# Optimization experiments

Hardware: AMD Instinct MI355X
Metric: run time of the kernel (lower is better)

## Reference

```python
import jax, jax.numpy as jnp
import numpy as np

N_HEADS, D_MODEL, D_HEAD = 16, 1024, 64
BATCH, SEQ = 8, 1024
INIT_RANGE = 0.02
IGNORE = -100000.0


def setup_inputs() -> dict:
    key = jax.random.key(0)
    ks = jax.random.split(key, 6)
    return {
        "normalized_resid_pre": jax.random.normal(ks[0], (BATCH, SEQ, D_MODEL), jnp.float32),
        "encoder_output": jax.random.normal(ks[1], (BATCH, SEQ, D_MODEL), jnp.float32),
        "Qs": jax.random.normal(ks[2], (N_HEADS, D_MODEL, D_HEAD), jnp.float32) * INIT_RANGE,
        "Qbs": jnp.zeros((N_HEADS, D_HEAD), jnp.float32),
        "Ks": jax.random.normal(ks[3], (N_HEADS, D_MODEL, D_HEAD), jnp.float32) * INIT_RANGE,
        "Kbs": jnp.zeros((N_HEADS, D_HEAD), jnp.float32),
        "Vs": jax.random.normal(ks[4], (N_HEADS, D_MODEL, D_HEAD), jnp.float32) * INIT_RANGE,
        "Vbs": jnp.zeros((N_HEADS, D_HEAD), jnp.float32),
        "O": jax.random.normal(ks[5], (N_HEADS, D_HEAD, D_MODEL), jnp.float32) * INIT_RANGE,
        "Ob": jnp.zeros((D_MODEL,), jnp.float32),
    }


def reference(normalized_resid_pre, encoder_output, Qs, Qbs, Ks, Kbs, Vs, Vbs, O, Ob):
    sqrt_d_head = np.sqrt(D_HEAD).astype(np.float32)
    # per-head projections: q,k from encoder_output, v from normalized_resid_pre
    q = jnp.einsum('bpd,hdk->bphk', encoder_output, Qs) + Qbs
    k = jnp.einsum('bpd,hdk->bphk', encoder_output, Ks) + Kbs
    v = jnp.einsum('bpd,hdk->bphk', normalized_resid_pre, Vs) + Vbs
    # [B,H,Q,K] scores, scaled then causally masked with -1e5 (not -inf)
    scores = jnp.einsum('bqhk,bmhk->bhqm', q, k) / sqrt_d_head
    causal = jnp.triu(jnp.ones((SEQ, SEQ), bool), k=1)
    scores = jnp.where(causal, jnp.float32(IGNORE), scores)
    attn = jax.nn.softmax(scores, axis=-1)
    z = jnp.einsum('bmhk,bhqm->bqhk', v, attn)
    return jnp.einsum('bqhk,hkd->bqd', z, O) + Ob
```

## Files before the change

### kernel.cpp

```cpp
#include <hip/hip_runtime.h>
#include <hip/hip_bf16.h>
#include <cstdint>
#include <cstddef>
#include <math.h>


typedef __attribute__((ext_vector_type(8))) short short8;
typedef __attribute__((ext_vector_type(4))) short short4v;
typedef __attribute__((ext_vector_type(4))) float f32x4;

#define MFMA16(A, B, C) __builtin_amdgcn_mfma_f32_16x16x32_bf16(A, B, C, 0, 0, 0)

__device__ inline short f2bs(float f) {
    __bf16 h = (__bf16)f;
    return __builtin_bit_cast(short, h);
}

typedef const __attribute__((address_space(1))) unsigned int* as1_u32p;
typedef __attribute__((address_space(3))) unsigned int* as3_u32p;

__device__ inline void gload_lds16(const void* g, void* lds_base) {
    __builtin_amdgcn_global_load_lds((as1_u32p)(uintptr_t)g,
                                     (as3_u32p)(uintptr_t)lds_base, 16, 0, 0);
}

__global__ __launch_bounds__(256) void cvt_k(const float* __restrict__ a,
                                             const float* __restrict__ b,
                                             short* __restrict__ oa,
                                             short* __restrict__ ob) {
    const int n = 8 * 1024 * 1024;
    const float* src = blockIdx.y ? b : a;
    short* dst = blockIdx.y ? ob : oa;
    for (int i = (blockIdx.x * 256 + threadIdx.x) * 8; i < n; i += gridDim.x * 256 * 8) {
        f32x4 v0 = *(const f32x4*)(src + i), v1 = *(const f32x4*)(src + i + 4);
        short8 o;
        o[0] = f2bs(v0[0]); o[1] = f2bs(v0[1]); o[2] = f2bs(v0[2]); o[3] = f2bs(v0[3]);
        o[4] = f2bs(v1[0]); o[5] = f2bs(v1[1]); o[6] = f2bs(v1[2]); o[7] = f2bs(v1[3]);
        *(short8*)(dst + i) = o;
    }
}

__global__ __launch_bounds__(256) void wtrans_k(
    const float* __restrict__ Wq, const float* __restrict__ Wk,
    const float* __restrict__ Wv, const float* __restrict__ Wo,
    short* __restrict__ TQ, short* __restrict__ TK,
    short* __restrict__ TV, short* __restrict__ TO) {
    __shared__ short tile[64][72];
    const int wsel = blockIdx.y;
    const float* in = wsel == 0 ? Wq : wsel == 1 ? Wk : wsel == 2 ? Wv : Wo;
    short* out = wsel == 0 ? TQ : wsel == 1 ? TK : wsel == 2 ? TV : TO;
    const int h = blockIdx.x >> 4, tk = blockIdx.x & 15;
    const int t = threadIdx.x;
    size_t ioff; int istr, orow0, ocol0;
    if (wsel < 3) { ioff = (size_t)h * 65536 + (size_t)tk * 64 * 64; istr = 64;   orow0 = h * 64;  ocol0 = tk * 64; }
    else          { ioff = (size_t)h * 65536 + (size_t)tk * 64;      istr = 1024; orow0 = tk * 64; ocol0 = h * 64; }
    {
        const int r = t >> 2, c0 = (t & 3) * 16;
        const float* src = in + ioff + (size_t)r * istr + c0;
#pragma unroll
        for (int j = 0; j < 4; j++) {
            f32x4 v = *(const f32x4*)(src + j * 4);
            tile[r][c0 + j * 4 + 0] = f2bs(v[0]);
            tile[r][c0 + j * 4 + 1] = f2bs(v[1]);
            tile[r][c0 + j * 4 + 2] = f2bs(v[2]);
            tile[r][c0 + j * 4 + 3] = f2bs(v[3]);
        }
    }
    __syncthreads();
    {
        const int cc = t >> 2, rb = (t & 3) * 16;
        short8 o0, o1;
#pragma unroll
        for (int j = 0; j < 8; j++) { o0[j] = tile[rb + j][cc]; o1[j] = tile[rb + 8 + j][cc]; }
        short* dst = out + (size_t)(orow0 + cc) * 1024 + ocol0 + rb;
        *(short8*)dst = o0;
        *(short8*)(dst + 8) = o1;
    }
}

template <int MODE>
__global__ __launch_bounds__(256) void gemm_bt(const short* __restrict__ A,
                                               const short* __restrict__ B,
                                               const float* __restrict__ bias,
                                               void* __restrict__ Cp,
                                               const float* __restrict__ bias2,
                                               void* __restrict__ Cp2) {
    constexpr int K = 1024;
    __shared__ short As[128 * 64];
    __shared__ short Bs[128 * 64];
    const int t = threadIdx.x, l = t & 63, w = t >> 6, lr = l & 15, lg = l >> 4;
    const int wm = (w >> 1) * 64, wn = (w & 1) * 64;
    const int m0 = blockIdx.x * 128, n0 = blockIdx.y * 128;
    const int sr = l >> 3, cb = l & 7;
    f32x4 acc[4][4] = {};

    for (int k0 = 0; k0 < K; k0 += 64) {
#pragma unroll
        for (int i = 0; i < 4; i++) {
            const int c = w * 4 + i, r = c * 8 + sr, cbs = cb ^ (r & 7);
            gload_lds16(A + (size_t)(m0 + r) * K + k0 + cbs * 8, &As[c * 512]);
        }
#pragma unroll
        for (int i = 0; i < 4; i++) {
            const int c = w * 4 + i, r = c * 8 + sr, cbs = cb ^ (r & 7);
            gload_lds16(B + (size_t)(n0 + r) * K + k0 + cbs * 8, &Bs[c * 512]);
        }
        __syncthreads();
#pragma unroll
        for (int kk = 0; kk < 2; kk++) {
            short8 af[4], bf[4];
#pragma unroll
            for (int mi = 0; mi < 4; mi++) {
                const int r = wm + mi * 16 + lr;
                af[mi] = *(const short8*)&As[r * 64 + ((kk * 4 + lg) ^ (r & 7)) * 8];
            }
#pragma unroll
            for (int nj = 0; nj < 4; nj++) {
                const int r = wn + nj * 16 + lr;
                bf[nj] = *(const short8*)&Bs[r * 64 + ((kk * 4 + lg) ^ (r & 7)) * 8];
            }
#pragma unroll
            for (int mi = 0; mi < 4; mi++)
#pragma unroll
                for (int nj = 0; nj < 4; nj++)
                    acc[mi][nj] = MFMA16(af[mi], bf[nj], acc[mi][nj]);
        }
        __syncthreads();
    }

#pragma unroll
    for (int mi = 0; mi < 4; mi++) {
#pragma unroll
        for (int nj = 0; nj < 4; nj++) {
            const int col = n0 + wn + nj * 16 + lr;
            if (MODE == 3) {
                const int h2 = col >> 6;
                short* dst = (short*)(h2 < 16 ? Cp : Cp2);
                const float bv = h2 < 16 ? bias[col & 1023] : bias2[col & 1023];
                const int h = h2 & 15, d = col & 63;
#pragma unroll
                for (int e = 0; e < 4; e++) {
                    const int row = m0 + wm + mi * 16 + lg * 4 + e;
                    const int bb = row >> 10, s = row & 1023;
                    dst[((size_t)(bb * 16 + h) * 1024 + s) * 64 + d] =
                        f2bs(acc[mi][nj][e] + bv);
                }
            } else if (MODE == 2) {
                const float bv = bias[col];
                const int rowb = m0 + wm + mi * 16 + lg * 4;
                const int bb = rowb >> 10, s0 = rowb & 1023;
                const int h = col >> 6, d = col & 63;
                short4v pk;
#pragma unroll
                for (int e = 0; e < 4; e++) pk[e] = f2bs(acc[mi][nj][e] + bv);
                *(short4v*)((short*)Cp + ((size_t)(bb * 16 + h) * 64 + d) * 1024 + s0) = pk;
            } else {
                const float bv = bias[col];
#pragma unroll
                for (int e = 0; e < 4; e++) {
                    const int row = m0 + wm + mi * 16 + lg * 4 + e;
                    ((float*)Cp)[(size_t)row * 1024 + col] = acc[mi][nj][e] + bv;
                }
            }
        }
    }
}

#define ATTN_THR 11.5415603f

__device__ __forceinline__ void attn_tile(
    const short* __restrict__ Ks, const short* __restrict__ Vt,
    short (*__restrict__ Psw)[76],
    const short8* __restrict__ qf, float* __restrict__ m,
    float* __restrict__ ps, f32x4* __restrict__ acc,
    bool diag, int lr, int lg, int rowloc) {
    f32x4 sf[4];
#pragma unroll
    for (int n = 0; n < 4; n++) {
        const int rk = n * 16 + lr;
        short8 kf0 = *(const short8*)&Ks[rk * 64 + ((lg) ^ (rk & 7)) * 8];
        short8 kf1 = *(const short8*)&Ks[rk * 64 + ((4 + lg) ^ (rk & 7)) * 8];
        f32x4 s = {};
        s = MFMA16(qf[0], kf0, s);
        s = MFMA16(qf[1], kf1, s);
        sf[n] = s;
    }
    const float SC = 0.18033688f;
#pragma unroll
    for (int n = 0; n < 4; n++)
#pragma unroll
        for (int e = 0; e < 4; e++) {
            float x = sf[n][e] * SC;
            if (diag && (n * 16 + lr > rowloc + e)) x = -1e30f;
            sf[n][e] = x;
        }
    float pm[4];
#pragma unroll
    for (int e = 0; e < 4; e++)
        pm[e] = fmaxf(fmaxf(sf[0][e], sf[1][e]), fmaxf(sf[2][e], sf[3][e]));
    bool ok = true;
#pragma unroll
    for (int e = 0; e < 4; e++) ok = ok && (pm[e] <= m[e] + ATTN_THR);
    if (!__all(ok)) {
#pragma unroll
        for (int e = 0; e < 4; e++) {
            float tm = pm[e];
#pragma unroll
            for (int off = 1; off < 16; off <<= 1)
                tm = fmaxf(tm, __shfl_xor(tm, off));
            float nm = fmaxf(m[e], tm);
            float al = exp2f(m[e] - nm);
            m[e] = nm;
            ps[e] *= al;
#pragma unroll
            for (int n4 = 0; n4 < 4; n4++) acc[n4][e] *= al;
        }
    }
#pragma unroll
    for (int e = 0; e < 4; e++) {
#pragma unroll
        for (int n = 0; n < 4; n++) {
            float p = exp2f(sf[n][e] - m[e]);
            ps[e] += p;
            Psw[lg * 4 + e][n * 16 + lr] = f2bs(p);
        }
    }
#pragma unroll
    for (int c = 0; c < 2; c++) {
        short8 pf = *(const short8*)&Psw[lr][lg * 8 + c * 32];
#pragma unroll
        for (int n4 = 0; n4 < 4; n4++) {
            const int rv = n4 * 16 + lr;
            short8 vf = *(const short8*)&Vt[rv * 64 + ((lg + 4 * c) ^ (rv & 7)) * 8];
            acc[n4] = MFMA16(pf, vf, acc[n4]);
        }
    }
}

__global__ __launch_bounds__(256, 4) void attn_k(const short* __restrict__ Q,
                                                 const short* __restrict__ Kp,
                                                 const short* __restrict__ Vg,
                                                 short* __restrict__ Z) {
    __shared__ short Ks[64 * 64];
    __shared__ short Vt[64 * 64];
    __shared__ short Ps[4][16][76];
    const int t = threadIdx.x, l = t & 63, w = t >> 6, lr = l & 15, lg = l >> 4;
    const int bh = blockIdx.x;
    const int qbA = blockIdx.y, qbB = 15 - qbA;
    const int q0A = qbA * 64, q0B = qbB * 64;
    const size_t base = (size_t)bh * 65536;
    const int sr = l >> 3, cb = l & 7;
    const int rowloc = w * 16 + lg * 4;

    short8 qfA[2], qfB[2];
    {
        const short* qp = Q + base + (size_t)(q0A + w * 16 + lr) * 64 + lg * 8;
        qfA[0] = *(const short8*)qp;
        qfA[1] = *(const short8*)(qp + 32);
        qp = Q + base + (size_t)(q0B + w * 16 + lr) * 64 + lg * 8;
        qfB[0] = *(const short8*)qp;
        qfB[1] = *(const short8*)(qp + 32);
    }

    float mA[4], mB[4], psA[4], psB[4];
    f32x4 accA[4] = {}, accB[4] = {};
#pragma unroll
    for (int e = 0; e < 4; e++) { mA[e] = mB[e] = -1e30f; psA[e] = psB[e] = 0.f; }

    for (int kt = 0; kt <= qbB; kt++) {
        const int k0 = kt * 64;
#pragma unroll
        for (int i = 0; i < 2; i++) {
            const int c = w * 2 + i, r = c * 8 + sr, cbs = cb ^ (r & 7);
            gload_lds16(Kp + base + (size_t)(k0 + r) * 64 + cbs * 8, &Ks[c * 512]);
            gload_lds16(Vg + base + (size_t)r * 1024 + k0 + cbs * 8, &Vt[c * 512]);
        }
        __syncthreads();
        if (kt <= qbA)
            attn_tile(Ks, Vt, Ps[w], qfA, mA, psA, accA, kt == qbA, lr, lg, rowloc);
        attn_tile(Ks, Vt, Ps[w], qfB, mB, psB, accB, kt == qbB, lr, lg, rowloc);
        __syncthreads();
    }

    const int b = bh >> 4, h = bh & 15;
#pragma unroll
    for (int e = 0; e < 4; e++) {
        float sA = psA[e], sB = psB[e];
#pragma unroll
        for (int off = 1; off < 16; off <<= 1) {
            sA += __shfl_xor(sA, off);
            sB += __shfl_xor(sB, off);
        }
        psA[e] = 1.f / sA;
        psB[e] = 1.f / sB;
    }
#pragma unroll
    for (int n4 = 0; n4 < 4; n4++)
#pragma unroll
        for (int e = 0; e < 4; e++) {
            const int rloc = w * 16 + lg * 4 + e;
            Z[((size_t)(b * 1024 + q0A + rloc)) * 1024 + h * 64 + n4 * 16 + lr] =
                f2bs(accA[n4][e] * psA[e]);
            Z[((size_t)(b * 1024 + q0B + rloc)) * 1024 + h * 64 + n4 * 16 + lr] =
                f2bs(accB[n4][e] * psB[e]);
        }
}

extern "C" void kernel_launch(void* const* d_in, const int* in_sizes, int n_in,
                              void* d_out, int out_size, void* d_ws, size_t ws_size,
                              hipStream_t stream) {
    const float* resid = (const float*)d_in[0];
    const float* enc   = (const float*)d_in[1];
    const float* Qs    = (const float*)d_in[2];
    const float* Qbs   = (const float*)d_in[3];
    const float* Ksw   = (const float*)d_in[4];
    const float* Kbs   = (const float*)d_in[5];
    const float* Vs    = (const float*)d_in[6];
    const float* Vbs   = (const float*)d_in[7];
    const float* Ow    = (const float*)d_in[8];
    const float* Ob    = (const float*)d_in[9];
    float* out = (float*)d_out;

    char* ws = (char*)d_ws;
    const size_t M16 = (size_t)16 * 1024 * 1024;
    short* Aenc = (short*)ws;
    short* Ares = (short*)(ws + M16);
    short* Qw   = (short*)(ws + 2 * M16);
    short* Kw   = (short*)(ws + 3 * M16);
    short* Vw   = (short*)(ws + 4 * M16);
    short* WqT  = (short*)(ws + 5 * M16);
    short* WkT  = (short*)(ws + 5 * M16 + 2 * 1024 * 1024);
    short* WvT  = (short*)(ws + 5 * M16 + 4 * 1024 * 1024);
    short* WoT  = (short*)(ws + 5 * M16 + 6 * 1024 * 1024);
    short* Zw   = Aenc;

    cvt_k<<<dim3(2048, 2), 256, 0, stream>>>(enc, resid, Aenc, Ares);
    wtrans_k<<<dim3(256, 4), 256, 0, stream>>>(Qs, Ksw, Vs, Ow, WqT, WkT, WvT, WoT);
    gemm_bt<3><<<dim3(64, 16), 256, 0, stream>>>(Aenc, WqT, Qbs, Qw, Kbs, Kw);
    gemm_bt<2><<<dim3(64, 8), 256, 0, stream>>>(Ares, WvT, Vbs, Vw, nullptr, nullptr);
    attn_k<<<dim3(128, 8), 256, 0, stream>>>(Qw, Kw, Vw, Zw);
    gemm_bt<0><<<dim3(64, 8), 256, 0, stream>>>(Zw, WoT, Ob, out, nullptr, nullptr);
}
```

Measured before the change: 169.6 us.

## Split paired query tiles into separate attention blocks and fold scale into Q

The attention kernel stops pairing a short and a long causal query tile in one block. It now launches one block per 64-row query tile, doubling the grid and raising the occupancy hint from 4 to 6 blocks per CU. The softmax scale is folded into the Q projection epilogue, and the diagonal mask is made a template parameter so non-diagonal tiles skip the scale and mask loop. This aims to improve parallelism and cut per-tile ALU work. In exchange, blocks become unbalanced, with K/V tiles loaded once per query tile instead of shared across two, and Q rounds to bf16 after scaling.

```diff
diff --git a/kernel.cpp b/kernel.cpp
--- a/kernel.cpp
+++ b/kernel.cpp
@@ -23,6 +23,9 @@
     __builtin_amdgcn_global_load_lds((as1_u32p)(uintptr_t)g,
                                      (as3_u32p)(uintptr_t)lds_base, 16, 0, 0);
 }
+
+#define ATTN_SC 0.18033688f
+#define ATTN_THR 11.5415603f
 
 __global__ __launch_bounds__(256) void cvt_k(const float* __restrict__ a,
                                              const float* __restrict__ b,
@@ -137,13 +140,14 @@
                 const int h2 = col >> 6;
                 short* dst = (short*)(h2 < 16 ? Cp : Cp2);
                 const float bv = h2 < 16 ? bias[col & 1023] : bias2[col & 1023];
+                const float sc = h2 < 16 ? ATTN_SC : 1.0f;
                 const int h = h2 & 15, d = col & 63;
 #pragma unroll
                 for (int e = 0; e < 4; e++) {
                     const int row = m0 + wm + mi * 16 + lg * 4 + e;
                     const int bb = row >> 10, s = row & 1023;
                     dst[((size_t)(bb * 16 + h) * 1024 + s) * 64 + d] =
-                        f2bs(acc[mi][nj][e] + bv);
+                        f2bs((acc[mi][nj][e] + bv) * sc);
                 }
             } else if (MODE == 2) {
                 const float bv = bias[col];
@@ -166,14 +170,13 @@
     }
 }
 
-#define ATTN_THR 11.5415603f
-
+template <bool DIAG>
 __device__ __forceinline__ void attn_tile(
     const short* __restrict__ Ks, const short* __restrict__ Vt,
     short (*__restrict__ Psw)[76],
     const short8* __restrict__ qf, float* __restrict__ m,
     float* __restrict__ ps, f32x4* __restrict__ acc,
-    bool diag, int lr, int lg, int rowloc) {
+    int lr, int lg, int rowloc) {
     f32x4 sf[4];
 #pragma unroll
     for (int n = 0; n < 4; n++) {
@@ -185,15 +188,13 @@
         s = MFMA16(qf[1], kf1, s);
         sf[n] = s;
     }
-    const float SC = 0.18033688f;
-#pragma unroll
-    for (int n = 0; n < 4; n++)
-#pragma unroll
-        for (int e = 0; e < 4; e++) {
-            float x = sf[n][e] * SC;
-            if (diag && (n * 16 + lr > rowloc + e)) x = -1e30f;
-            sf[n][e] = x;
-        }
+    if (DIAG) {
+#pragma unroll
+        for (int n = 0; n < 4; n++)
+#pragma unroll
+            for (int e = 0; e < 4; e++)
+                if (n * 16 + lr > rowloc + e) sf[n][e] = -1e30f;
+    }
     float pm[4];
 #pragma unroll
     for (int e = 0; e < 4; e++)
@@ -237,7 +238,7 @@
     }
 }
 
-__global__ __launch_bounds__(256, 4) void attn_k(const short* __restrict__ Q,
+__global__ __launch_bounds__(256, 6) void attn_k(const short* __restrict__ Q,
                                                  const short* __restrict__ Kp,
                                                  const short* __restrict__ Vg,
                                                  short* __restrict__ Z) {
@@ -246,28 +247,25 @@
     __shared__ short Ps[4][16][76];
     const int t = threadIdx.x, l = t & 63, w = t >> 6, lr = l & 15, lg = l >> 4;
     const int bh = blockIdx.x;
-    const int qbA = blockIdx.y, qbB = 15 - qbA;
-    const int q0A = qbA * 64, q0B = qbB * 64;
+    const int qb = 15 - blockIdx.y;
+    const int q0 = qb * 64;
     const size_t base = (size_t)bh * 65536;
     const int sr = l >> 3, cb = l & 7;
     const int rowloc = w * 16 + lg * 4;
 
-    short8 qfA[2], qfB[2];
+    short8 qf[2];
     {
-        const short* qp = Q + base + (size_t)(q0A + w * 16 + lr) * 64 + lg * 8;
-        qfA[0] = *(const short8*)qp;
-        qfA[1] = *(const short8*)(qp + 32);
-        qp = Q + base + (size_t)(q0B + w * 16 + lr) * 64 + lg * 8;
-        qfB[0] = *(const short8*)qp;
-        qfB[1] = *(const short8*)(qp + 32);
-    }
-
-    float mA[4], mB[4], psA[4], psB[4];
-    f32x4 accA[4] = {}, accB[4] = {};
-#pragma unroll
-    for (int e = 0; e < 4; e++) { mA[e] = mB[e] = -1e30f; psA[e] = psB[e] = 0.f; }
-
-    for (int kt = 0; kt <= qbB; kt++) {
+        const short* qp = Q + base + (size_t)(q0 + w * 16 + lr) * 64 + lg * 8;
+        qf[0] = *(const short8*)qp;
+        qf[1] = *(const short8*)(qp + 32);
+    }
+
+    float m[4], ps[4];
+    f32x4 acc[4] = {};
+#pragma unroll
+    for (int e = 0; e < 4; e++) { m[e] = -1e30f; ps[e] = 0.f; }
+
+    for (int kt = 0; kt <= qb; kt++) {
         const int k0 = kt * 64;
 #pragma unroll
         for (int i = 0; i < 2; i++) {
@@ -276,33 +274,28 @@
             gload_lds16(Vg + base + (size_t)r * 1024 + k0 + cbs * 8, &Vt[c * 512]);
         }
         __syncthreads();
-        if (kt <= qbA)
-            attn_tile(Ks, Vt, Ps[w], qfA, mA, psA, accA, kt == qbA, lr, lg, rowloc);
-        attn_tile(Ks, Vt, Ps[w], qfB, mB, psB, accB, kt == qbB, lr, lg, rowloc);
+        if (kt == qb)
+            attn_tile<true>(Ks, Vt, Ps[w], qf, m, ps, acc, lr, lg, rowloc);
+        else
+            attn_tile<false>(Ks, Vt, Ps[w], qf, m, ps, acc, lr, lg, rowloc);
         __syncthreads();
     }
 
     const int b = bh >> 4, h = bh & 15;
 #pragma unroll
     for (int e = 0; e < 4; e++) {
-        float sA = psA[e], sB = psB[e];
-#pragma unroll
-        for (int off = 1; off < 16; off <<= 1) {
-            sA += __shfl_xor(sA, off);
-            sB += __shfl_xor(sB, off);
-        }
-        psA[e] = 1.f / sA;
-        psB[e] = 1.f / sB;
+        float s = ps[e];
+#pragma unroll
+        for (int off = 1; off < 16; off <<= 1) s += __shfl_xor(s, off);
+        ps[e] = 1.f / s;
     }
 #pragma unroll
     for (int n4 = 0; n4 < 4; n4++)
 #pragma unroll
         for (int e = 0; e < 4; e++) {
             const int rloc = w * 16 + lg * 4 + e;
-            Z[((size_t)(b * 1024 + q0A + rloc)) * 1024 + h * 64 + n4 * 16 + lr] =
-                f2bs(accA[n4][e] * psA[e]);
-            Z[((size_t)(b * 1024 + q0B + rloc)) * 1024 + h * 64 + n4 * 16 + lr] =
-                f2bs(accB[n4][e] * psB[e]);
+            Z[((size_t)(b * 1024 + q0 + rloc)) * 1024 + h * 64 + n4 * 16 + lr] =
+                f2bs(acc[n4][e] * ps[e]);
         }
 }
 
@@ -338,6 +331,6 @@
     wtrans_k<<<dim3(256, 4), 256, 0, stream>>>(Qs, Ksw, Vs, Ow, WqT, WkT, WvT, WoT);
     gemm_bt<3><<<dim3(64, 16), 256, 0, stream>>>(Aenc, WqT, Qbs, Qw, Kbs, Kw);
     gemm_bt<2><<<dim3(64, 8), 256, 0, stream>>>(Ares, WvT, Vbs, Vw, nullptr, nullptr);
-    attn_k<<<dim3(128, 8), 256, 0, stream>>>(Qw, Kw, Vw, Zw);
+    attn_k<<<dim3(128, 16), 256, 0, stream>>>(Qw, Kw, Vw, Zw);
     gemm_bt<0><<<dim3(64, 8), 256, 0, stream>>>(Zw, WoT, Ob, out, nullptr, nullptr);
 }
```

After: 196.3 us. 1.16x slower.
